# Performance work log

Measured on AMD Instinct MI355X. Metric: run time of the kernel, lower is better.

## Reference

```python
import jax, jax.numpy as jnp
import numpy as np

E = 1024   # embd_size
H = 16     # head_count
HS = E // H
B = 8
T = 1024   # seq len == input_size
EPS = 1e-5

def _ln(x, g, b):
    m = jnp.mean(x, axis=-1, keepdims=True)
    v = jnp.mean((x - m) ** 2, axis=-1, keepdims=True)
    return (x - m) * jax.lax.rsqrt(v + EPS) * g + b

def setup_inputs() -> dict:
    key = jax.random.key(0)
    ks = jax.random.split(key, 12)
    s_attn = 1.0 / np.sqrt(E)
    s_ff1 = 1.0 / np.sqrt(E)
    s_ff2 = 1.0 / np.sqrt(4 * E)
    return {
        "x": jax.random.normal(ks[0], (B, T, E), dtype=jnp.float32),
        "wq": jax.random.normal(ks[1], (H, E, HS), dtype=jnp.float32) * s_attn,
        "wk": jax.random.normal(ks[2], (H, E, HS), dtype=jnp.float32) * s_attn,
        "wv": jax.random.normal(ks[3], (H, E, HS), dtype=jnp.float32) * s_attn,
        "w_proj": jax.random.normal(ks[4], (E, E), dtype=jnp.float32) * s_attn,
        "b_proj": jnp.zeros((E,), dtype=jnp.float32),
        "w1": jax.random.normal(ks[5], (E, 4 * E), dtype=jnp.float32) * s_ff1,
        "b1": jnp.zeros((4 * E,), dtype=jnp.float32),
        "w2": jax.random.normal(ks[6], (4 * E, E), dtype=jnp.float32) * s_ff2,
        "b2": jnp.zeros((E,), dtype=jnp.float32),
        "g1": jnp.ones((E,), dtype=jnp.float32),
        "be1": jnp.zeros((E,), dtype=jnp.float32),
        "g2": jnp.ones((E,), dtype=jnp.float32),
        "be2": jnp.zeros((E,), dtype=jnp.float32),
    }

def reference(x, wq, wk, wv, w_proj, b_proj, w1, b1, w2, b2, g1, be1, g2, be2):
    Tn = x.shape[1]
    h = _ln(x, g1, be1)
    # per-head projections, batched over heads: [B,T,E] x [H,E,S] -> [B,H,T,S]
    q = jnp.einsum('bte,hes->bhts', h, wq)
    k = jnp.einsum('bte,hes->bhts', h, wk)
    v = jnp.einsum('bte,hes->bhts', h, wv)
    scores = jnp.einsum('bhts,bhus->bhtu', q, k)
    # NOTE: source multiplies by sqrt(T) (x.shape[2] of scores), not 1/sqrt(head_size)
    scores = scores * jnp.float32(Tn) ** 0.5
    causal = jnp.tril(jnp.ones((Tn, Tn), dtype=bool))
    scores = jnp.where(causal, scores, -jnp.inf)
    attn = jax.nn.softmax(scores, axis=-1)
    out = jnp.einsum('bhtu,bhus->bhts', attn, v)           # [B,H,T,S]
    out = out.transpose(0, 2, 1, 3).reshape(x.shape[0], Tn, E)  # concat heads
    out = out @ w_proj + b_proj
    x = x + out
    f = _ln(x, g2, be2)
    f = jax.nn.relu(f @ w1 + b1) @ w2 + b2
    return x + f
```

## Files before the change

kernel.cpp:

```cpp
#include <hip/hip_runtime.h>


typedef unsigned short u16;
typedef __attribute__((ext_vector_type(8))) short  bfx8;
typedef __attribute__((ext_vector_type(4))) float  f32x4;
typedef __attribute__((ext_vector_type(4))) unsigned short u16v4;

#define MFMA16 __builtin_amdgcn_mfma_f32_16x16x32_bf16

__device__ __forceinline__ u16 f2bf(float f) {
    union { float f; unsigned u; } c; c.f = f;
    unsigned r = c.u + 0x7fffu + ((c.u >> 16) & 1u);
    return (u16)(r >> 16);
}
__device__ __forceinline__ float bf2f(u16 b) {
    union { unsigned u; float f; } c; c.u = ((unsigned)b) << 16; return c.f;
}
__device__ __forceinline__ float exp2_fast(float x) {
    float r; asm("v_exp_f32 %0, %1" : "=v"(r) : "v"(x)); return r;
}

__device__ __forceinline__ void gl_lds16(const void* g, void* l) {
    void* gg = (void*)g;
    __builtin_amdgcn_global_load_lds(
        (__attribute__((address_space(1))) void*)gg,
        (__attribute__((address_space(3))) void*)l,
        16, 0, 0);
}

__global__ __launch_bounds__(256)
void transpose_split(const float* __restrict__ src, u16* __restrict__ dhi,
                     u16* __restrict__ dlo, int C, int OS,
                     size_t inBS, size_t outBS)
{
    __shared__ float t[64][65];
    const int tid = threadIdx.x;
    const float* s = src + (size_t)blockIdx.z * inBS
                   + ((size_t)blockIdx.y * 64) * C + (size_t)blockIdx.x * 64;
    const size_t obase = (size_t)blockIdx.z * outBS
                       + ((size_t)blockIdx.x * 64) * OS + (size_t)blockIdx.y * 64;
    {
        const int r = tid >> 2, c4 = (tid & 3) * 16;
#pragma unroll
        for (int k = 0; k < 4; ++k) {
            float4 f = *(const float4*)(s + (size_t)r * C + c4 + k * 4);
            t[r][c4 + k*4 + 0] = f.x; t[r][c4 + k*4 + 1] = f.y;
            t[r][c4 + k*4 + 2] = f.z; t[r][c4 + k*4 + 3] = f.w;
        }
    }
    __syncthreads();
    {
        const int c = tid >> 2, r4 = (tid & 3) * 16;
        bfx8 h0, h1, l0, l1;
#pragma unroll
        for (int k = 0; k < 8; ++k) {
            float v0 = t[r4 + k][c];
            float v1 = t[r4 + 8 + k][c];
            u16 a = f2bf(v0), b = f2bf(v1);
            h0[k] = (short)a; h1[k] = (short)b;
            l0[k] = (short)f2bf(v0 - bf2f(a));
            l1[k] = (short)f2bf(v1 - bf2f(b));
        }
        u16* d = dhi + obase + (size_t)c * OS + r4;
        *(bfx8*)d = h0; *(bfx8*)(d + 8) = h1;
        if (dlo) {
            u16* d2 = dlo + obase + (size_t)c * OS + r4;
            *(bfx8*)d2 = l0; *(bfx8*)(d2 + 8) = l1;
        }
    }
}

__global__ __launch_bounds__(256)
void transpose_v(const u16* __restrict__ v, u16* __restrict__ vT)
{
    const int ut = blockIdx.x, h = blockIdx.y, b = blockIdx.z;
    __shared__ u16 t[64][72];
    const int tid = threadIdx.x;
    {
        const int u = tid >> 2, s4 = (tid & 3) * 16;
        const u16* src = v + ((size_t)(b * 1024 + ut * 64 + u)) * 1024 + h * 64 + s4;
        bfx8 a = *(const bfx8*)src;
        bfx8 c = *(const bfx8*)(src + 8);
#pragma unroll
        for (int k = 0; k < 8; ++k) { t[u][s4 + k] = (u16)a[k]; t[u][s4 + 8 + k] = (u16)c[k]; }
    }
    __syncthreads();
    {
        const int s = tid >> 2, u4 = (tid & 3) * 16;
        bfx8 o0, o1;
#pragma unroll
        for (int k = 0; k < 8; ++k) { o0[k] = (short)t[u4 + k][s]; o1[k] = (short)t[u4 + 8 + k][s]; }
        u16* dst = vT + ((size_t)((b * 16 + h) * 64 + s)) * 1024 + ut * 64 + u4;
        *(bfx8*)dst = o0; *(bfx8*)(dst + 8) = o1;
    }
}

__global__ __launch_bounds__(256)
void ln_split(const float* __restrict__ x, const float* __restrict__ g,
              const float* __restrict__ be, u16* __restrict__ hhi,
              u16* __restrict__ hlo)
{
    const int row = blockIdx.x;
    const int tid = threadIdx.x;
    const float4 v = ((const float4*)(x + (size_t)row * 1024))[tid];
    float s  = v.x + v.y + v.z + v.w;
    float s2 = v.x*v.x + v.y*v.y + v.z*v.z + v.w*v.w;
#pragma unroll
    for (int m = 32; m >= 1; m >>= 1) {
        s  += __shfl_xor(s,  m, 64);
        s2 += __shfl_xor(s2, m, 64);
    }
    __shared__ float rs[4], rq[4];
    if ((tid & 63) == 0) { rs[tid >> 6] = s; rq[tid >> 6] = s2; }
    __syncthreads();
    s  = rs[0] + rs[1] + rs[2] + rs[3];
    s2 = rq[0] + rq[1] + rq[2] + rq[3];
    const float mean = s * (1.0f / 1024.0f);
    const float var  = s2 * (1.0f / 1024.0f) - mean * mean;
    const float inv  = rsqrtf(var + 1e-5f);
    const int col0 = tid * 4;
    float hv[4];
    hv[0] = (v.x - mean) * inv * g[col0+0] + be[col0+0];
    hv[1] = (v.y - mean) * inv * g[col0+1] + be[col0+1];
    hv[2] = (v.z - mean) * inv * g[col0+2] + be[col0+2];
    hv[3] = (v.w - mean) * inv * g[col0+3] + be[col0+3];
    u16v4 hb, lb;
#pragma unroll
    for (int k = 0; k < 4; ++k) {
        u16 a = f2bf(hv[k]);
        hb[k] = a;
        lb[k] = f2bf(hv[k] - bf2f(a));
    }
    *(u16v4*)(hhi + (size_t)row * 1024 + col0) = hb;
    if (hlo) *(u16v4*)(hlo + (size_t)row * 1024 + col0) = lb;
}

#define BM 128
#define BN 128
#define BKT 32

template<int FLAGS>
__global__ __launch_bounds__(256, 2)
void gemm_bt(const u16* __restrict__ A, const u16* __restrict__ Bt,
             void* __restrict__ Cout, const float* __restrict__ bias,
             const float* __restrict__ res, int M, int N, int K)
{
    __shared__ u16 As[BM * BKT];
    __shared__ u16 Bs[BN * BKT];
    const int tid  = threadIdx.x;
    const int lane = tid & 63, wave = tid >> 6;
    const int wr = wave >> 1, wc = wave & 1;
    const int li = lane & 15, lg = lane >> 4;
    const size_t m0 = (size_t)blockIdx.y * BM;
    const size_t n0 = (size_t)blockIdx.x * BN;
    f32x4 acc[4][4] = {};

    const int slot0 = tid, slot1 = tid + 256;
    const int r0 = slot0 >> 2, kc0 = (slot0 & 3) * 8;
    const int r1 = slot1 >> 2, kc1 = (slot1 & 3) * 8;

    for (int kt = 0; kt < K; kt += BKT) {
        __syncthreads();
        gl_lds16(A  + (m0 + r0) * K + kt + kc0, As + slot0 * 8);
        gl_lds16(Bt + (n0 + r0) * K + kt + kc0, Bs + slot0 * 8);
        gl_lds16(A  + (m0 + r1) * K + kt + kc1, As + slot1 * 8);
        gl_lds16(Bt + (n0 + r1) * K + kt + kc1, Bs + slot1 * 8);
        __syncthreads();
        bfx8 af[4], bfr[4];
#pragma unroll
        for (int i = 0; i < 4; ++i)
            af[i] = *(const bfx8*)&As[(wr * 64 + i * 16 + li) * BKT + lg * 8];
#pragma unroll
        for (int j = 0; j < 4; ++j)
            bfr[j] = *(const bfx8*)&Bs[(wc * 64 + j * 16 + li) * BKT + lg * 8];
#pragma unroll
        for (int i = 0; i < 4; ++i)
#pragma unroll
            for (int j = 0; j < 4; ++j)
                acc[i][j] = MFMA16(af[i], bfr[j], acc[i][j], 0, 0, 0);
    }

    float* Cf = (float*)Cout;
    u16*   Cb = (u16*)Cout;
#pragma unroll
    for (int i = 0; i < 4; ++i)
#pragma unroll
        for (int j = 0; j < 4; ++j)
#pragma unroll
            for (int r = 0; r < 4; ++r) {
                const size_t row = m0 + wr * 64 + i * 16 + lg * 4 + r;
                const size_t col = n0 + wc * 64 + j * 16 + li;
                float v = acc[i][j][r];
                if (FLAGS & 1) v += bias[col];
                if (FLAGS & 2) v = fmaxf(v, 0.0f);
                if (FLAGS & 4) v += res[row * (size_t)N + col];
                if (FLAGS & 8) Cf[row * (size_t)N + col] = v;
                else           Cb[row * (size_t)N + col] = f2bf(v);
            }
}

__global__ __launch_bounds__(512, 2)
void gemm8_ffn1(const u16* __restrict__ A, const u16* __restrict__ Bt,
                u16* __restrict__ C, const float* __restrict__ bias,
                int M, int N, int K)
{
    __shared__ u16 Asl[2][2][128 * 64];
    __shared__ u16 Bsl[2][2][128 * 64];
    const int tid = threadIdx.x;
    const int lane = tid & 63, wave = tid >> 6;
    const int wr = wave >> 2, wc = wave & 3;
    const int li = lane & 15, lg = lane >> 4;

    const int bid = blockIdx.x;
    const int swz = (bid & 7) * 64 + (bid >> 3);
    const int bx = swz & 15, by = swz >> 4;
    const size_t m0 = (size_t)by * 256, n0 = (size_t)bx * 256;

    char* ldsA = (char*)&Asl[0][0][0];
    char* ldsB = (char*)&Bsl[0][0][0];

    auto stageA = [&](int j, int h) {
#pragma unroll
        for (int site = 0; site < 2; ++site) {
            const int s = tid + site * 512;
            const int r = s >> 3;
            const int cb = ((s & 7) << 4) ^ ((r & 7) << 4);
            gl_lds16((const char*)(A + (m0 + h * 128 + r) * (size_t)K + (size_t)j * 64) + cb,
                     ldsA + ((j & 1) * 2 + h) * 16384 + s * 16);
        }
    };
    auto stageB = [&](int j, int h) {
#pragma unroll
        for (int site = 0; site < 2; ++site) {
            const int s = tid + site * 512;
            const int r = s >> 3;
            const int cb = ((s & 7) << 4) ^ ((r & 7) << 4);
            gl_lds16((const char*)(Bt + (n0 + h * 128 + r) * (size_t)K + (size_t)j * 64) + cb,
                     ldsB + ((j & 1) * 2 + h) * 16384 + s * 16);
        }
    };

    const int lsw = (li & 7) << 4;
    const int aHalfBase = wr * 16384;
    const int bHalfBase = (wc >> 1) * 16384;
    const int bRow0 = (wc & 1) * 64;

    f32x4 acc[8][4] = {};
    const int NT = K >> 6;
    const int NI = NT >> 1;

    stageA(0, 0); stageA(0, 1); stageB(0, 0); stageB(0, 1);
    stageB(1, 0); stageB(1, 1);
    asm volatile("s_waitcnt vmcnt(0)" ::: "memory");
    __builtin_amdgcn_sched_barrier(0);
    __builtin_amdgcn_s_barrier();
    __builtin_amdgcn_sched_barrier(0);

    for (int t = 0; t < NI; ++t) {
        const bool more = (t + 1 < NI);
#pragma unroll
        for (int half = 0; half < 2; ++half) {
            const int buf = half;
            const int abase = buf * 32768 + aHalfBase;
            const int bbase = buf * 32768 + bHalfBase;
            bfx8 bfr[4][2];
#pragma unroll
            for (int q = 0; q < 4; ++q) {
                if (q == 0) {
#pragma unroll
                    for (int nf = 0; nf < 4; ++nf)
#pragma unroll
                        for (int ks = 0; ks < 2; ++ks)
                            bfr[nf][ks] = *(const bfx8*)(ldsB + bbase
                                + (bRow0 + nf * 16 + li) * 128
                                + ((ks * 64 + lg * 16) ^ lsw));
                }
                bfx8 afr[2][2];
#pragma unroll
                for (int m = 0; m < 2; ++m)
#pragma unroll
                    for (int ks = 0; ks < 2; ++ks)
                        afr[m][ks] = *(const bfx8*)(ldsA + abase
                            + ((2 * q + m) * 16 + li) * 128
                            + ((ks * 64 + lg * 16) ^ lsw));

                if (half == 0) {
                    if (q == 0) stageA(2 * t + 1, 0);
                    else if (q == 1) stageA(2 * t + 1, 1);
                    else if (q == 2) { if (more) stageB(2 * t + 2, 0); }
                    else             { if (more) stageB(2 * t + 2, 1); }
                } else {
                    if (q == 0)      { if (more) stageA(2 * t + 2, 0); }
                    else if (q == 1) { if (more) stageA(2 * t + 2, 1); }
                    else if (q == 2) { if (more) stageB(2 * t + 3, 0); }
                    else             { if (more) stageB(2 * t + 3, 1); }
                }

                __builtin_amdgcn_sched_barrier(0);
                __builtin_amdgcn_s_barrier();
                asm volatile("s_waitcnt lgkmcnt(0)" ::: "memory");
                __builtin_amdgcn_sched_barrier(0);
                __builtin_amdgcn_s_setprio(1);
#pragma unroll
                for (int ks = 0; ks < 2; ++ks)
#pragma unroll
                    for (int m = 0; m < 2; ++m)
#pragma unroll
                        for (int nf = 0; nf < 4; ++nf)
                            acc[2 * q + m][nf] = MFMA16(afr[m][ks], bfr[nf][ks],
                                                        acc[2 * q + m][nf], 0, 0, 0);
                __builtin_amdgcn_s_setprio(0);
                __builtin_amdgcn_sched_barrier(0);
                if (q == 3) {
                    if (half == 0) {
                        if (more) { asm volatile("s_waitcnt vmcnt(4)" ::: "memory"); }
                        else      { asm volatile("s_waitcnt vmcnt(0)" ::: "memory"); }
                    } else if (more) {
                        asm volatile("s_waitcnt vmcnt(4)" ::: "memory");
                    }
                    __builtin_amdgcn_sched_barrier(0);
                }
                __builtin_amdgcn_s_barrier();
                __builtin_amdgcn_sched_barrier(0);
            }
        }
    }

#pragma unroll
    for (int i = 0; i < 8; ++i)
#pragma unroll
        for (int nf = 0; nf < 4; ++nf)
#pragma unroll
            for (int r = 0; r < 4; ++r) {
                const size_t row = m0 + wr * 128 + i * 16 + lg * 4 + r;
                const size_t col = n0 + wc * 64 + nf * 16 + li;
                float v = acc[i][nf][r] + bias[col];
                v = fmaxf(v, 0.0f);
                C[row * (size_t)N + col] = f2bf(v);
            }
}

__global__ __launch_bounds__(256, 2)
void gemm_qk(const u16* __restrict__ Ah, const u16* __restrict__ Al,
             const u16* __restrict__ Bh, const u16* __restrict__ Bl,
             u16* __restrict__ Ohi, u16* __restrict__ Olo,
             int M, int N, int K)
{
    __shared__ u16 Ahs[BM * BKT], Als[BM * BKT], Bhs[BN * BKT], Bls[BN * BKT];
    const int tid  = threadIdx.x;
    const int lane = tid & 63, wave = tid >> 6;
    const int wr = wave >> 1, wc = wave & 1;
    const int li = lane & 15, lg = lane >> 4;
    const size_t m0 = (size_t)blockIdx.y * BM;
    const size_t n0 = (size_t)blockIdx.x * BN;
    f32x4 acc[4][4] = {};

    const int slot0 = tid, slot1 = tid + 256;
    const int r0 = slot0 >> 2, kc0 = (slot0 & 3) * 8;
    const int r1 = slot1 >> 2, kc1 = (slot1 & 3) * 8;

    for (int kt = 0; kt < K; kt += BKT) {
        __syncthreads();
        gl_lds16(Ah + (m0 + r0) * K + kt + kc0, Ahs + slot0 * 8);
        gl_lds16(Al + (m0 + r0) * K + kt + kc0, Als + slot0 * 8);
        gl_lds16(Bh + (n0 + r0) * K + kt + kc0, Bhs + slot0 * 8);
        gl_lds16(Bl + (n0 + r0) * K + kt + kc0, Bls + slot0 * 8);
        gl_lds16(Ah + (m0 + r1) * K + kt + kc1, Ahs + slot1 * 8);
        gl_lds16(Al + (m0 + r1) * K + kt + kc1, Als + slot1 * 8);
        gl_lds16(Bh + (n0 + r1) * K + kt + kc1, Bhs + slot1 * 8);
        gl_lds16(Bl + (n0 + r1) * K + kt + kc1, Bls + slot1 * 8);
        __syncthreads();
        bfx8 ah[4], al4[4], bh[4], bl4[4];
#pragma unroll
        for (int i = 0; i < 4; ++i) {
            ah[i]  = *(const bfx8*)&Ahs[(wr * 64 + i * 16 + li) * BKT + lg * 8];
            al4[i] = *(const bfx8*)&Als[(wr * 64 + i * 16 + li) * BKT + lg * 8];
        }
#pragma unroll
        for (int j = 0; j < 4; ++j) {
            bh[j]  = *(const bfx8*)&Bhs[(wc * 64 + j * 16 + li) * BKT + lg * 8];
            bl4[j] = *(const bfx8*)&Bls[(wc * 64 + j * 16 + li) * BKT + lg * 8];
        }
#pragma unroll
        for (int i = 0; i < 4; ++i)
#pragma unroll
            for (int j = 0; j < 4; ++j) {
                acc[i][j] = MFMA16(ah[i],  bh[j],  acc[i][j], 0, 0, 0);
                acc[i][j] = MFMA16(ah[i],  bl4[j], acc[i][j], 0, 0, 0);
                acc[i][j] = MFMA16(al4[i], bh[j],  acc[i][j], 0, 0, 0);
            }
    }
#pragma unroll
    for (int i = 0; i < 4; ++i)
#pragma unroll
        for (int j = 0; j < 4; ++j)
#pragma unroll
            for (int r = 0; r < 4; ++r) {
                const size_t row = m0 + wr * 64 + i * 16 + lg * 4 + r;
                const size_t col = n0 + wc * 64 + j * 16 + li;
                const float v = acc[i][j][r];
                const u16 hi = f2bf(v);
                Ohi[row * (size_t)N + col] = hi;
                Olo[row * (size_t)N + col] = f2bf(v - bf2f(hi));
            }
}

__global__ __launch_bounds__(256, 3)
void attn(const u16* __restrict__ qhi, const u16* __restrict__ qlo,
          const u16* __restrict__ khi, const u16* __restrict__ klo,
          const u16* __restrict__ vt, u16* __restrict__ ao)
{
    const int id  = blockIdx.x;
    const int swz = (id & 7) * 256 + (id >> 3);
    const int qt  = 15 - (swz & 15);
    const int h   = (swz >> 4) & 15;
    const int b   = swz >> 8;

    const int tid = threadIdx.x;
    const int wave = tid >> 6, lane = tid & 63;
    const int li = lane & 15, lg = lane >> 4;

    __shared__ u16 KsHi[2][4096];
    __shared__ u16 KsLo[2][4096];
    __shared__ u16 Pl[64 * 72];

    const size_t qrow = (size_t)b * 1024 + qt * 64 + wave * 16 + li;
    const size_t qoff = qrow * 1024 + h * 64 + lg * 8;
    const bfx8 qh0 = *(const bfx8*)(qhi + qoff);
    const bfx8 qh1 = *(const bfx8*)(qhi + qoff + 32);
    const bfx8 ql0 = *(const bfx8*)(qlo + qoff);
    const bfx8 ql1 = *(const bfx8*)(qlo + qoff + 32);

    bfx8 onesf;
#pragma unroll
    for (int k = 0; k < 8; ++k) onesf[k] = (short)0x3F80;

    f32x4 O[4] = {};
    f32x4 O5 = {0.f, 0.f, 0.f, 0.f};
    float mrow[4] = {-3e38f, -3e38f, -3e38f, -3e38f};

    const u16* kh_base = khi + ((size_t)b * 1024) * 1024 + h * 64;
    const u16* kl_base = klo + ((size_t)b * 1024) * 1024 + h * 64;
    const u16* v_base  = vt + ((size_t)(b * 16 + h) * 64) * 1024;

    auto stageK = [&](int kt, int bufIdx) {
#pragma unroll
        for (int site = 0; site < 2; ++site) {
            const int s = tid + site * 256;
            const int r = s >> 3;
            const int cb = (((s & 7) << 4) ^ ((r & 7) << 4));
            const size_t go = ((size_t)(kt * 64 + r)) * 1024;
            gl_lds16((const char*)(kh_base + go) + cb, (char*)&KsHi[bufIdx][0] + s * 16);
            gl_lds16((const char*)(kl_base + go) + cb, (char*)&KsLo[bufIdx][0] + s * 16);
        }
    };

    const int rswz = (li & 7) << 4;

    stageK(0, 0);

    for (int kt = 0; kt <= qt; ++kt) {
        const int cur = kt & 1;

        bfx8 vld[2][4];
#pragma unroll
        for (int nf = 0; nf < 4; ++nf) {
            const u16* vr = v_base + ((size_t)(nf * 16 + li)) * 1024 + kt * 64 + lg * 8;
            vld[0][nf] = *(const bfx8*)vr;
            vld[1][nf] = *(const bfx8*)(vr + 32);
        }

        if (kt < qt) {
            stageK(kt + 1, cur ^ 1);
            asm volatile("s_waitcnt vmcnt(12)" ::: "memory");
        } else {
            asm volatile("s_waitcnt vmcnt(8)" ::: "memory");
        }
        __builtin_amdgcn_sched_barrier(0);
        __builtin_amdgcn_s_barrier();
        __builtin_amdgcn_sched_barrier(0);

        float sv[4][4];
        const char* khc = (const char*)&KsHi[cur][0];
        const char* klc = (const char*)&KsLo[cur][0];
#pragma unroll
        for (int nf = 0; nf < 4; ++nf) {
            const int rb = (nf * 16 + li) * 128;
            bfx8 kh0v = *(const bfx8*)(khc + rb + (((lg * 16) + 0 ) ^ rswz));
            bfx8 kh1v = *(const bfx8*)(khc + rb + (((lg * 16) + 64) ^ rswz));
            bfx8 kl0v = *(const bfx8*)(klc + rb + (((lg * 16) + 0 ) ^ rswz));
            bfx8 kl1v = *(const bfx8*)(klc + rb + (((lg * 16) + 64) ^ rswz));
            f32x4 a = {0.f, 0.f, 0.f, 0.f};
            a = MFMA16(qh0, kh0v, a, 0, 0, 0);
            a = MFMA16(qh1, kh1v, a, 0, 0, 0);
            a = MFMA16(qh0, kl0v, a, 0, 0, 0);
            a = MFMA16(qh1, kl1v, a, 0, 0, 0);
            a = MFMA16(ql0, kh0v, a, 0, 0, 0);
            a = MFMA16(ql1, kh1v, a, 0, 0, 0);
#pragma unroll
            for (int r = 0; r < 4; ++r) sv[nf][r] = a[r];
        }

        asm volatile("s_waitcnt lgkmcnt(0)" ::: "memory");
        __builtin_amdgcn_sched_barrier(0);
        __builtin_amdgcn_s_barrier();
        __builtin_amdgcn_sched_barrier(0);

        const float SC = 46.16624130844683f;
        float pmax[4] = {-3e38f, -3e38f, -3e38f, -3e38f};
        if (kt == qt) {
            const int rowg = qt * 64 + wave * 16 + lg * 4;
            const int colg = kt * 64 + li;
#pragma unroll
            for (int nf = 0; nf < 4; ++nf)
#pragma unroll
                for (int r = 0; r < 4; ++r) {
                    float x2 = sv[nf][r] * SC;
                    if (colg + nf * 16 > rowg + r) x2 = -3e38f;
                    sv[nf][r] = x2;
                    pmax[r] = fmaxf(pmax[r], x2);
                }
        } else {
#pragma unroll
            for (int nf = 0; nf < 4; ++nf)
#pragma unroll
                for (int r = 0; r < 4; ++r) {
                    const float x2 = sv[nf][r] * SC;
                    sv[nf][r] = x2;
                    pmax[r] = fmaxf(pmax[r], x2);
                }
        }
#pragma unroll
        for (int msk = 1; msk < 16; msk <<= 1)
#pragma unroll
            for (int r = 0; r < 4; ++r)
                pmax[r] = fmaxf(pmax[r], __shfl_xor(pmax[r], msk, 64));

        const bool grow = !__all((pmax[0] - mrow[0] <= 11.5416f) &&
                                 (pmax[1] - mrow[1] <= 11.5416f) &&
                                 (pmax[2] - mrow[2] <= 11.5416f) &&
                                 (pmax[3] - mrow[3] <= 11.5416f));
        if (grow) {
            float alr[4];
#pragma unroll
            for (int r = 0; r < 4; ++r) {
                const float mnew = fmaxf(mrow[r], pmax[r]);
                alr[r] = exp2_fast(mrow[r] - mnew);
                mrow[r] = mnew;
            }
#pragma unroll
            for (int nf = 0; nf < 4; ++nf)
#pragma unroll
                for (int r = 0; r < 4; ++r)
                    O[nf][r] *= alr[r];
#pragma unroll
            for (int r = 0; r < 4; ++r)
                O5[r] *= alr[r];
        }

#pragma unroll
        for (int nf = 0; nf < 4; ++nf)
#pragma unroll
            for (int r = 0; r < 4; ++r)
                Pl[(wave * 16 + lg * 4 + r) * 72 + nf * 16 + li] =
                    f2bf(exp2_fast(sv[nf][r] - mrow[r]));

#pragma unroll
        for (int ku = 0; ku < 2; ++ku) {
            bfx8 pf = *(const bfx8*)&Pl[(wave * 16 + li) * 72 + ku * 32 + lg * 8];
#pragma unroll
            for (int nf = 0; nf < 4; ++nf)
                O[nf] = MFMA16(pf, vld[ku][nf], O[nf], 0, 0, 0);
            O5 = MFMA16(pf, onesf, O5, 0, 0, 0);
        }
    }

    float invl[4];
#pragma unroll
    for (int r = 0; r < 4; ++r) invl[r] = 1.0f / O5[r];
    const size_t orow = (size_t)b * 1024 + qt * 64 + wave * 16 + lg * 4;
#pragma unroll
    for (int nf = 0; nf < 4; ++nf)
#pragma unroll
        for (int r = 0; r < 4; ++r)
            ao[(orow + r) * 1024 + h * 64 + nf * 16 + li] = f2bf(O[nf][r] * invl[r]);
}

extern "C" void kernel_launch(void* const* d_in, const int* in_sizes, int n_in,
                              void* d_out, int out_size, void* d_ws, size_t ws_size,
                              hipStream_t stream)
{
    (void)in_sizes; (void)n_in; (void)out_size; (void)ws_size;
    const float* x      = (const float*)d_in[0];
    const float* wq     = (const float*)d_in[1];
    const float* wk     = (const float*)d_in[2];
    const float* wv     = (const float*)d_in[3];
    const float* w_proj = (const float*)d_in[4];
    const float* b_proj = (const float*)d_in[5];
    const float* w1     = (const float*)d_in[6];
    const float* b1     = (const float*)d_in[7];
    const float* w2     = (const float*)d_in[8];
    const float* b2     = (const float*)d_in[9];
    const float* g1     = (const float*)d_in[10];
    const float* be1    = (const float*)d_in[11];
    const float* g2     = (const float*)d_in[12];
    const float* be2    = (const float*)d_in[13];
    float* out = (float*)d_out;

    const size_t ME2 = (size_t)8192 * 1024 * 2;
    char* wsp = (char*)d_ws;
    u16* h_hi = (u16*)(wsp + 0 * ME2);
    u16* h_lo = (u16*)(wsp + 1 * ME2);
    u16* q_hi = (u16*)(wsp + 2 * ME2);
    u16* q_lo = (u16*)(wsp + 3 * ME2);
    u16* k_hi = (u16*)(wsp + 4 * ME2);
    u16* k_lo = (u16*)(wsp + 5 * ME2);
    u16* v_b  = (u16*)(wsp + 6 * ME2);
    u16* vtr  = (u16*)(wsp + 7 * ME2);
    float* y  = (float*)(wsp + 8 * ME2);
    char* wp0 = wsp + 8 * ME2 + (size_t)8192 * 1024 * 4;
    const size_t W1M = (size_t)1024 * 1024 * 2;
    u16* wqT_hi = (u16*)(wp0 + 0 * W1M);
    u16* wqT_lo = (u16*)(wp0 + 1 * W1M);
    u16* wkT_hi = (u16*)(wp0 + 2 * W1M);
    u16* wkT_lo = (u16*)(wp0 + 3 * W1M);
    u16* wvT    = (u16*)(wp0 + 4 * W1M);
    u16* wpT    = (u16*)(wp0 + 5 * W1M);
    u16* w1T    = (u16*)(wp0 + 6 * W1M);
    u16* w2T    = (u16*)(wp0 + 6 * W1M + 4 * W1M);
    u16* f2  = h_hi;
    u16* ao  = h_lo;
    u16* act = q_hi;

    dim3 blk(256);

    transpose_split<<<dim3(1, 16, 16), blk, 0, stream>>>(wq, wqT_hi, wqT_lo, 64, 1024, (size_t)65536, (size_t)65536);
    transpose_split<<<dim3(1, 16, 16), blk, 0, stream>>>(wk, wkT_hi, wkT_lo, 64, 1024, (size_t)65536, (size_t)65536);
    transpose_split<<<dim3(1, 16, 16), blk, 0, stream>>>(wv, wvT, nullptr, 64, 1024, (size_t)65536, (size_t)65536);
    transpose_split<<<dim3(16, 16, 1), blk, 0, stream>>>(w_proj, wpT, nullptr, 1024, 1024, 0, 0);
    transpose_split<<<dim3(64, 16, 1), blk, 0, stream>>>(w1, w1T, nullptr, 4096, 1024, 0, 0);
    transpose_split<<<dim3(16, 64, 1), blk, 0, stream>>>(w2, w2T, nullptr, 1024, 4096, 0, 0);

    ln_split<<<8192, blk, 0, stream>>>(x, g1, be1, h_hi, h_lo);

    gemm_qk<<<dim3(8, 64), blk, 0, stream>>>(h_hi, h_lo, wqT_hi, wqT_lo, q_hi, q_lo, 8192, 1024, 1024);
    gemm_qk<<<dim3(8, 64), blk, 0, stream>>>(h_hi, h_lo, wkT_hi, wkT_lo, k_hi, k_lo, 8192, 1024, 1024);
    gemm_bt<0><<<dim3(8, 64), blk, 0, stream>>>(h_hi, wvT, v_b, nullptr, nullptr, 8192, 1024, 1024);
    transpose_v<<<dim3(16, 16, 8), blk, 0, stream>>>(v_b, vtr);

    attn<<<dim3(2048), blk, 0, stream>>>(q_hi, q_lo, k_hi, k_lo, vtr, ao);

    gemm_bt<1 | 4 | 8><<<dim3(8, 64), blk, 0, stream>>>(ao, wpT, y, b_proj, x, 8192, 1024, 1024);

    ln_split<<<8192, blk, 0, stream>>>(y, g2, be2, f2, nullptr);

    gemm8_ffn1<<<dim3(512), dim3(512), 0, stream>>>(f2, w1T, act, b1, 8192, 4096, 1024);
    gemm_bt<1 | 4 | 8><<<dim3(8, 64), blk, 0, stream>>>(act, w2T, out, b2, y, 8192, 1024, 4096);
}
```

Before: 539.0 us.

## Enlarge attention query tile to 128 rows with 8 waves sharing K stages

The attention kernel now uses 512-thread blocks covering 128 query rows (8 waves), so each staged K tile in LDS is reused by twice as many query rows and grid size halves. Waves whose rows lie entirely above a key tile skip the QK and PV work for that tile but still join the barriers. The P buffer becomes a per-wave XOR-swizzled band to reduce LDS bank conflicts. In exchange there is more per-block LDS, idle waves on diagonal tiles, and fewer blocks for load balancing.

Measured after the change: 961.9 us. +78.5%, slower.

```diff
diff --git a/kernel.cpp b/kernel.cpp
--- a/kernel.cpp
+++ b/kernel.cpp
@@ -405,16 +405,16 @@
             }
 }
 
-__global__ __launch_bounds__(256, 3)
+__global__ __launch_bounds__(512, 6)
 void attn(const u16* __restrict__ qhi, const u16* __restrict__ qlo,
           const u16* __restrict__ khi, const u16* __restrict__ klo,
           const u16* __restrict__ vt, u16* __restrict__ ao)
 {
     const int id  = blockIdx.x;
-    const int swz = (id & 7) * 256 + (id >> 3);
-    const int qt  = 15 - (swz & 15);
-    const int h   = (swz >> 4) & 15;
-    const int b   = swz >> 8;
+    const int swz = (id & 7) * 128 + (id >> 3);
+    const int qt  = 7 - (swz & 7);
+    const int h   = (swz >> 3) & 15;
+    const int b   = swz >> 7;
 
     const int tid = threadIdx.x;
     const int wave = tid >> 6, lane = tid & 63;
@@ -422,9 +422,9 @@
 
     __shared__ u16 KsHi[2][4096];
     __shared__ u16 KsLo[2][4096];
-    __shared__ u16 Pl[64 * 72];
-
-    const size_t qrow = (size_t)b * 1024 + qt * 64 + wave * 16 + li;
+    __shared__ u16 Pl[8][1024];
+
+    const size_t qrow = (size_t)b * 1024 + qt * 128 + wave * 16 + li;
     const size_t qoff = qrow * 1024 + h * 64 + lg * 8;
     const bfx8 qh0 = *(const bfx8*)(qhi + qoff);
     const bfx8 qh1 = *(const bfx8*)(qhi + qoff + 32);
@@ -444,23 +444,25 @@
     const u16* v_base  = vt + ((size_t)(b * 16 + h) * 64) * 1024;
 
     auto stageK = [&](int kt, int bufIdx) {
-#pragma unroll
-        for (int site = 0; site < 2; ++site) {
-            const int s = tid + site * 256;
-            const int r = s >> 3;
-            const int cb = (((s & 7) << 4) ^ ((r & 7) << 4));
-            const size_t go = ((size_t)(kt * 64 + r)) * 1024;
-            gl_lds16((const char*)(kh_base + go) + cb, (char*)&KsHi[bufIdx][0] + s * 16);
-            gl_lds16((const char*)(kl_base + go) + cb, (char*)&KsLo[bufIdx][0] + s * 16);
-        }
+        const int s = tid;
+        const int r = s >> 3;
+        const int cb = (((s & 7) << 4) ^ ((r & 7) << 4));
+        const size_t go = ((size_t)(kt * 64 + r)) * 1024;
+        gl_lds16((const char*)(kh_base + go) + cb, (char*)&KsHi[bufIdx][0] + s * 16);
+        gl_lds16((const char*)(kl_base + go) + cb, (char*)&KsLo[bufIdx][0] + s * 16);
     };
 
     const int rswz = (li & 7) << 4;
-
+    const int rmin = qt * 128 + wave * 16;
+    char* pband = (char*)&Pl[wave][0];
+
+    const int nkt = 2 * qt + 2;
     stageK(0, 0);
 
-    for (int kt = 0; kt <= qt; ++kt) {
+    for (int kt = 0; kt < nkt; ++kt) {
         const int cur = kt & 1;
+        const int colbase = kt * 64;
+        const bool skip = (colbase > rmin + 15);
 
         bfx8 vld[2][4];
 #pragma unroll
@@ -470,9 +472,9 @@
             vld[1][nf] = *(const bfx8*)(vr + 32);
         }
 
-        if (kt < qt) {
+        if (kt + 1 < nkt) {
             stageK(kt + 1, cur ^ 1);
-            asm volatile("s_waitcnt vmcnt(12)" ::: "memory");
+            asm volatile("s_waitcnt vmcnt(10)" ::: "memory");
         } else {
             asm volatile("s_waitcnt vmcnt(8)" ::: "memory");
         }
@@ -481,24 +483,26 @@
         __builtin_amdgcn_sched_barrier(0);
 
         float sv[4][4];
-        const char* khc = (const char*)&KsHi[cur][0];
-        const char* klc = (const char*)&KsLo[cur][0];
-#pragma unroll
-        for (int nf = 0; nf < 4; ++nf) {
-            const int rb = (nf * 16 + li) * 128;
-            bfx8 kh0v = *(const bfx8*)(khc + rb + (((lg * 16) + 0 ) ^ rswz));
-            bfx8 kh1v = *(const bfx8*)(khc + rb + (((lg * 16) + 64) ^ rswz));
-            bfx8 kl0v = *(const bfx8*)(klc + rb + (((lg * 16) + 0 ) ^ rswz));
-            bfx8 kl1v = *(const bfx8*)(klc + rb + (((lg * 16) + 64) ^ rswz));
-            f32x4 a = {0.f, 0.f, 0.f, 0.f};
-            a = MFMA16(qh0, kh0v, a, 0, 0, 0);
-            a = MFMA16(qh1, kh1v, a, 0, 0, 0);
-            a = MFMA16(qh0, kl0v, a, 0, 0, 0);
-            a = MFMA16(qh1, kl1v, a, 0, 0, 0);
-            a = MFMA16(ql0, kh0v, a, 0, 0, 0);
-            a = MFMA16(ql1, kh1v, a, 0, 0, 0);
-#pragma unroll
-            for (int r = 0; r < 4; ++r) sv[nf][r] = a[r];
+        if (!skip) {
+            const char* khc = (const char*)&KsHi[cur][0];
+            const char* klc = (const char*)&KsLo[cur][0];
+#pragma unroll
+            for (int nf = 0; nf < 4; ++nf) {
+                const int rb = (nf * 16 + li) * 128;
+                bfx8 kh0v = *(const bfx8*)(khc + rb + (((lg * 16) + 0 ) ^ rswz));
+                bfx8 kh1v = *(const bfx8*)(khc + rb + (((lg * 16) + 64) ^ rswz));
+                bfx8 kl0v = *(const bfx8*)(klc + rb + (((lg * 16) + 0 ) ^ rswz));
+                bfx8 kl1v = *(const bfx8*)(klc + rb + (((lg * 16) + 64) ^ rswz));
+                f32x4 a = {0.f, 0.f, 0.f, 0.f};
+                a = MFMA16(qh0, kh0v, a, 0, 0, 0);
+                a = MFMA16(qh1, kh1v, a, 0, 0, 0);
+                a = MFMA16(qh0, kl0v, a, 0, 0, 0);
+                a = MFMA16(qh1, kl1v, a, 0, 0, 0);
+                a = MFMA16(ql0, kh0v, a, 0, 0, 0);
+                a = MFMA16(ql1, kh1v, a, 0, 0, 0);
+#pragma unroll
+                for (int r = 0; r < 4; ++r) sv[nf][r] = a[r];
+            }
         }
 
         asm volatile("s_waitcnt lgkmcnt(0)" ::: "memory");
@@ -506,79 +510,85 @@
         __builtin_amdgcn_s_barrier();
         __builtin_amdgcn_sched_barrier(0);
 
-        const float SC = 46.16624130844683f;
-        float pmax[4] = {-3e38f, -3e38f, -3e38f, -3e38f};
-        if (kt == qt) {
-            const int rowg = qt * 64 + wave * 16 + lg * 4;
-            const int colg = kt * 64 + li;
+        if (!skip) {
+            const float SC = 46.16624130844683f;
+            float pmax[4] = {-3e38f, -3e38f, -3e38f, -3e38f};
+            const bool domask = (colbase + 63 > rmin);
+            if (domask) {
+                const int rowg = rmin + lg * 4;
+                const int colg = colbase + li;
+#pragma unroll
+                for (int nf = 0; nf < 4; ++nf)
+#pragma unroll
+                    for (int r = 0; r < 4; ++r) {
+                        float x2 = sv[nf][r] * SC;
+                        if (colg + nf * 16 > rowg + r) x2 = -3e38f;
+                        sv[nf][r] = x2;
+                        pmax[r] = fmaxf(pmax[r], x2);
+                    }
+            } else {
+#pragma unroll
+                for (int nf = 0; nf < 4; ++nf)
+#pragma unroll
+                    for (int r = 0; r < 4; ++r) {
+                        const float x2 = sv[nf][r] * SC;
+                        sv[nf][r] = x2;
+                        pmax[r] = fmaxf(pmax[r], x2);
+                    }
+            }
+#pragma unroll
+            for (int msk = 1; msk < 16; msk <<= 1)
+#pragma unroll
+                for (int r = 0; r < 4; ++r)
+                    pmax[r] = fmaxf(pmax[r], __shfl_xor(pmax[r], msk, 64));
+
+            const bool grow = !__all((pmax[0] - mrow[0] <= 11.5416f) &&
+                                     (pmax[1] - mrow[1] <= 11.5416f) &&
+                                     (pmax[2] - mrow[2] <= 11.5416f) &&
+                                     (pmax[3] - mrow[3] <= 11.5416f));
+            if (grow) {
+                float alr[4];
+#pragma unroll
+                for (int r = 0; r < 4; ++r) {
+                    const float mnew = fmaxf(mrow[r], pmax[r]);
+                    alr[r] = exp2_fast(mrow[r] - mnew);
+                    mrow[r] = mnew;
+                }
+#pragma unroll
+                for (int nf = 0; nf < 4; ++nf)
+#pragma unroll
+                    for (int r = 0; r < 4; ++r)
+                        O[nf][r] *= alr[r];
+#pragma unroll
+                for (int r = 0; r < 4; ++r)
+                    O5[r] *= alr[r];
+            }
+
 #pragma unroll
             for (int nf = 0; nf < 4; ++nf)
 #pragma unroll
                 for (int r = 0; r < 4; ++r) {
-                    float x2 = sv[nf][r] * SC;
-                    if (colg + nf * 16 > rowg + r) x2 = -3e38f;
-                    sv[nf][r] = x2;
-                    pmax[r] = fmaxf(pmax[r], x2);
+                    const int prow = lg * 4 + r;
+                    const int pb = prow * 128 + ((((nf * 16 + li) * 2)) ^ ((prow & 7) << 4));
+                    *(u16*)(pband + pb) = f2bf(exp2_fast(sv[nf][r] - mrow[r]));
                 }
-        } else {
-#pragma unroll
-            for (int nf = 0; nf < 4; ++nf)
-#pragma unroll
-                for (int r = 0; r < 4; ++r) {
-                    const float x2 = sv[nf][r] * SC;
-                    sv[nf][r] = x2;
-                    pmax[r] = fmaxf(pmax[r], x2);
-                }
-        }
-#pragma unroll
-        for (int msk = 1; msk < 16; msk <<= 1)
-#pragma unroll
-            for (int r = 0; r < 4; ++r)
-                pmax[r] = fmaxf(pmax[r], __shfl_xor(pmax[r], msk, 64));
-
-        const bool grow = !__all((pmax[0] - mrow[0] <= 11.5416f) &&
-                                 (pmax[1] - mrow[1] <= 11.5416f) &&
-                                 (pmax[2] - mrow[2] <= 11.5416f) &&
-                                 (pmax[3] - mrow[3] <= 11.5416f));
-        if (grow) {
-            float alr[4];
-#pragma unroll
-            for (int r = 0; r < 4; ++r) {
-                const float mnew = fmaxf(mrow[r], pmax[r]);
-                alr[r] = exp2_fast(mrow[r] - mnew);
-                mrow[r] = mnew;
-            }
-#pragma unroll
-            for (int nf = 0; nf < 4; ++nf)
-#pragma unroll
-                for (int r = 0; r < 4; ++r)
-                    O[nf][r] *= alr[r];
-#pragma unroll
-            for (int r = 0; r < 4; ++r)
-                O5[r] *= alr[r];
-        }
-
-#pragma unroll
-        for (int nf = 0; nf < 4; ++nf)
-#pragma unroll
-            for (int r = 0; r < 4; ++r)
-                Pl[(wave * 16 + lg * 4 + r) * 72 + nf * 16 + li] =
-                    f2bf(exp2_fast(sv[nf][r] - mrow[r]));
-
-#pragma unroll
-        for (int ku = 0; ku < 2; ++ku) {
-            bfx8 pf = *(const bfx8*)&Pl[(wave * 16 + li) * 72 + ku * 32 + lg * 8];
-#pragma unroll
-            for (int nf = 0; nf < 4; ++nf)
-                O[nf] = MFMA16(pf, vld[ku][nf], O[nf], 0, 0, 0);
-            O5 = MFMA16(pf, onesf, O5, 0, 0, 0);
+
+#pragma unroll
+            for (int ku = 0; ku < 2; ++ku) {
+                bfx8 pf = *(const bfx8*)(pband + li * 128
+                                         + ((ku * 64 + lg * 16) ^ ((li & 7) << 4)));
+#pragma unroll
+                for (int nf = 0; nf < 4; ++nf)
+                    O[nf] = MFMA16(pf, vld[ku][nf], O[nf], 0, 0, 0);
+                O5 = MFMA16(pf, onesf, O5, 0, 0, 0);
+            }
         }
     }
 
     float invl[4];
 #pragma unroll
     for (int r = 0; r < 4; ++r) invl[r] = 1.0f / O5[r];
-    const size_t orow = (size_t)b * 1024 + qt * 64 + wave * 16 + lg * 4;
+    const size_t orow = (size_t)b * 1024 + qt * 128 + wave * 16 + lg * 4;
 #pragma unroll
     for (int nf = 0; nf < 4; ++nf)
 #pragma unroll
@@ -648,7 +658,7 @@
     gemm_bt<0><<<dim3(8, 64), blk, 0, stream>>>(h_hi, wvT, v_b, nullptr, nullptr, 8192, 1024, 1024);
     transpose_v<<<dim3(16, 16, 8), blk, 0, stream>>>(v_b, vtr);
 
-    attn<<<dim3(2048), blk, 0, stream>>>(q_hi, q_lo, k_hi, k_lo, vtr, ao);
+    attn<<<dim3(1024), dim3(512), 0, stream>>>(q_hi, q_lo, k_hi, k_lo, vtr, ao);
 
     gemm_bt<1 | 4 | 8><<<dim3(8, 64), blk, 0, stream>>>(ao, wpT, y, b_proj, x, 8192, 1024, 1024);
 
```

## Fuse Q and K projections into one GEMM and swizzle attention P buffer

Applied to the files above, without the earlier changes.

Concatenates the transposed Q and K weights so a single gemm_qk launch produces an interleaved [8192,2048] QK output, and the attention kernel reads Q and K from it with a 2048 stride. The P staging buffer in LDS becomes unpadded 64x64 with an XOR swizzle per wave band, which shrinks shared memory, and launch bounds rise to 4 blocks per CU. The aim is to cut one kernel launch, improve GEMM occupancy across a wider N, and raise attention occupancy. The risk is register pressure from the higher occupancy bound, and wider-strided Q/K reads in attention.

Result: slower. 647.4 us (+20.1%).

```diff
diff --git a/kernel.cpp b/kernel.cpp
--- a/kernel.cpp
+++ b/kernel.cpp
@@ -405,9 +405,10 @@
             }
 }
 
-__global__ __launch_bounds__(256, 3)
-void attn(const u16* __restrict__ qhi, const u16* __restrict__ qlo,
-          const u16* __restrict__ khi, const u16* __restrict__ klo,
+#define QKS 2048
+
+__global__ __launch_bounds__(256, 4)
+void attn(const u16* __restrict__ qkhi, const u16* __restrict__ qklo,
           const u16* __restrict__ vt, u16* __restrict__ ao)
 {
     const int id  = blockIdx.x;
@@ -422,14 +423,14 @@
 
     __shared__ u16 KsHi[2][4096];
     __shared__ u16 KsLo[2][4096];
-    __shared__ u16 Pl[64 * 72];
+    __shared__ u16 Pl[64 * 64];
 
     const size_t qrow = (size_t)b * 1024 + qt * 64 + wave * 16 + li;
-    const size_t qoff = qrow * 1024 + h * 64 + lg * 8;
-    const bfx8 qh0 = *(const bfx8*)(qhi + qoff);
-    const bfx8 qh1 = *(const bfx8*)(qhi + qoff + 32);
-    const bfx8 ql0 = *(const bfx8*)(qlo + qoff);
-    const bfx8 ql1 = *(const bfx8*)(qlo + qoff + 32);
+    const size_t qoff = qrow * QKS + h * 64 + lg * 8;
+    const bfx8 qh0 = *(const bfx8*)(qkhi + qoff);
+    const bfx8 qh1 = *(const bfx8*)(qkhi + qoff + 32);
+    const bfx8 ql0 = *(const bfx8*)(qklo + qoff);
+    const bfx8 ql1 = *(const bfx8*)(qklo + qoff + 32);
 
     bfx8 onesf;
 #pragma unroll
@@ -439,8 +440,8 @@
     f32x4 O5 = {0.f, 0.f, 0.f, 0.f};
     float mrow[4] = {-3e38f, -3e38f, -3e38f, -3e38f};
 
-    const u16* kh_base = khi + ((size_t)b * 1024) * 1024 + h * 64;
-    const u16* kl_base = klo + ((size_t)b * 1024) * 1024 + h * 64;
+    const u16* kh_base = qkhi + ((size_t)b * 1024) * QKS + 1024 + h * 64;
+    const u16* kl_base = qklo + ((size_t)b * 1024) * QKS + 1024 + h * 64;
     const u16* v_base  = vt + ((size_t)(b * 16 + h) * 64) * 1024;
 
     auto stageK = [&](int kt, int bufIdx) {
@@ -449,13 +450,14 @@
             const int s = tid + site * 256;
             const int r = s >> 3;
             const int cb = (((s & 7) << 4) ^ ((r & 7) << 4));
-            const size_t go = ((size_t)(kt * 64 + r)) * 1024;
+            const size_t go = ((size_t)(kt * 64 + r)) * QKS;
             gl_lds16((const char*)(kh_base + go) + cb, (char*)&KsHi[bufIdx][0] + s * 16);
             gl_lds16((const char*)(kl_base + go) + cb, (char*)&KsLo[bufIdx][0] + s * 16);
         }
     };
 
     const int rswz = (li & 7) << 4;
+    char* pband = (char*)&Pl[0] + wave * 2048;
 
     stageK(0, 0);
 
@@ -561,13 +563,16 @@
 #pragma unroll
         for (int nf = 0; nf < 4; ++nf)
 #pragma unroll
-            for (int r = 0; r < 4; ++r)
-                Pl[(wave * 16 + lg * 4 + r) * 72 + nf * 16 + li] =
-                    f2bf(exp2_fast(sv[nf][r] - mrow[r]));
+            for (int r = 0; r < 4; ++r) {
+                const int prow = lg * 4 + r;
+                const int pb = prow * 128 + ((((nf * 16 + li) * 2)) ^ ((prow & 7) << 4));
+                *(u16*)(pband + pb) = f2bf(exp2_fast(sv[nf][r] - mrow[r]));
+            }
 
 #pragma unroll
         for (int ku = 0; ku < 2; ++ku) {
-            bfx8 pf = *(const bfx8*)&Pl[(wave * 16 + li) * 72 + ku * 32 + lg * 8];
+            bfx8 pf = *(const bfx8*)(pband + li * 128
+                                     + ((ku * 64 + lg * 16) ^ ((li & 7) << 4)));
 #pragma unroll
             for (int nf = 0; nf < 4; ++nf)
                 O[nf] = MFMA16(pf, vld[ku][nf], O[nf], 0, 0, 0);
@@ -607,35 +612,29 @@
     const float* be2    = (const float*)d_in[13];
     float* out = (float*)d_out;
 
-    const size_t ME2 = (size_t)8192 * 1024 * 2;
+    const size_t MB = (size_t)1024 * 1024;
     char* wsp = (char*)d_ws;
-    u16* h_hi = (u16*)(wsp + 0 * ME2);
-    u16* h_lo = (u16*)(wsp + 1 * ME2);
-    u16* q_hi = (u16*)(wsp + 2 * ME2);
-    u16* q_lo = (u16*)(wsp + 3 * ME2);
-    u16* k_hi = (u16*)(wsp + 4 * ME2);
-    u16* k_lo = (u16*)(wsp + 5 * ME2);
-    u16* v_b  = (u16*)(wsp + 6 * ME2);
-    u16* vtr  = (u16*)(wsp + 7 * ME2);
-    float* y  = (float*)(wsp + 8 * ME2);
-    char* wp0 = wsp + 8 * ME2 + (size_t)8192 * 1024 * 4;
-    const size_t W1M = (size_t)1024 * 1024 * 2;
-    u16* wqT_hi = (u16*)(wp0 + 0 * W1M);
-    u16* wqT_lo = (u16*)(wp0 + 1 * W1M);
-    u16* wkT_hi = (u16*)(wp0 + 2 * W1M);
-    u16* wkT_lo = (u16*)(wp0 + 3 * W1M);
-    u16* wvT    = (u16*)(wp0 + 4 * W1M);
-    u16* wpT    = (u16*)(wp0 + 5 * W1M);
-    u16* w1T    = (u16*)(wp0 + 6 * W1M);
-    u16* w2T    = (u16*)(wp0 + 6 * W1M + 4 * W1M);
+    u16* h_hi  = (u16*)(wsp + 0 * MB);
+    u16* h_lo  = (u16*)(wsp + 16 * MB);
+    u16* qk_hi = (u16*)(wsp + 32 * MB);
+    u16* qk_lo = (u16*)(wsp + 64 * MB);
+    u16* v_b   = (u16*)(wsp + 96 * MB);
+    u16* vtr   = (u16*)(wsp + 112 * MB);
+    float* y   = (float*)(wsp + 128 * MB);
+    u16* wqkT_hi = (u16*)(wsp + 160 * MB);
+    u16* wqkT_lo = (u16*)(wsp + 164 * MB);
+    u16* wvT     = (u16*)(wsp + 168 * MB);
+    u16* wpT     = (u16*)(wsp + 170 * MB);
+    u16* w1T     = (u16*)(wsp + 172 * MB);
+    u16* w2T     = (u16*)(wsp + 180 * MB);
     u16* f2  = h_hi;
     u16* ao  = h_lo;
-    u16* act = q_hi;
+    u16* act = qk_hi;
 
     dim3 blk(256);
 
-    transpose_split<<<dim3(1, 16, 16), blk, 0, stream>>>(wq, wqT_hi, wqT_lo, 64, 1024, (size_t)65536, (size_t)65536);
-    transpose_split<<<dim3(1, 16, 16), blk, 0, stream>>>(wk, wkT_hi, wkT_lo, 64, 1024, (size_t)65536, (size_t)65536);
+    transpose_split<<<dim3(1, 16, 16), blk, 0, stream>>>(wq, wqkT_hi, wqkT_lo, 64, 1024, (size_t)65536, (size_t)65536);
+    transpose_split<<<dim3(1, 16, 16), blk, 0, stream>>>(wk, wqkT_hi + (size_t)1024 * 1024, wqkT_lo + (size_t)1024 * 1024, 64, 1024, (size_t)65536, (size_t)65536);
     transpose_split<<<dim3(1, 16, 16), blk, 0, stream>>>(wv, wvT, nullptr, 64, 1024, (size_t)65536, (size_t)65536);
     transpose_split<<<dim3(16, 16, 1), blk, 0, stream>>>(w_proj, wpT, nullptr, 1024, 1024, 0, 0);
     transpose_split<<<dim3(64, 16, 1), blk, 0, stream>>>(w1, w1T, nullptr, 4096, 1024, 0, 0);
@@ -643,12 +642,11 @@
 
     ln_split<<<8192, blk, 0, stream>>>(x, g1, be1, h_hi, h_lo);
 
-    gemm_qk<<<dim3(8, 64), blk, 0, stream>>>(h_hi, h_lo, wqT_hi, wqT_lo, q_hi, q_lo, 8192, 1024, 1024);
-    gemm_qk<<<dim3(8, 64), blk, 0, stream>>>(h_hi, h_lo, wkT_hi, wkT_lo, k_hi, k_lo, 8192, 1024, 1024);
+    gemm_qk<<<dim3(16, 64), blk, 0, stream>>>(h_hi, h_lo, wqkT_hi, wqkT_lo, qk_hi, qk_lo, 8192, 2048, 1024);
     gemm_bt<0><<<dim3(8, 64), blk, 0, stream>>>(h_hi, wvT, v_b, nullptr, nullptr, 8192, 1024, 1024);
     transpose_v<<<dim3(16, 16, 8), blk, 0, stream>>>(v_b, vtr);
 
-    attn<<<dim3(2048), blk, 0, stream>>>(q_hi, q_lo, k_hi, k_lo, vtr, ao);
+    attn<<<dim3(2048), blk, 0, stream>>>(qk_hi, qk_lo, vtr, ao);
 
     gemm_bt<1 | 4 | 8><<<dim3(8, 64), blk, 0, stream>>>(ao, wpT, y, b_proj, x, 8192, 1024, 1024);
 
```
